# Kernel tuning notes

Measured on AMD Instinct MI355X. Metric: run time of the kernel, lower is better.

## Reference

```python
import jax, jax.numpy as jnp
import numpy as np

# Fixed problem geometry: B equal-sized graphs with contiguous node ids.
B, N, E, F_IN, H, C = 64, 1024, 655360, 128, 128, 10
K1 = int(np.ceil(0.8 * N))    # 820 nodes/graph kept by pool1
K2 = int(np.ceil(0.8 * K1))   # 656 nodes/graph kept by pool2


def setup_inputs() -> dict:
    key = jax.random.key(0)
    ks = jax.random.split(key, 12)
    x = jax.random.normal(ks[0], (B * N, F_IN), jnp.float32)
    # intra-graph random edges, E//B per graph
    e_per = E // B
    local = jax.random.randint(ks[1], (2, E), 0, N)
    off = jnp.repeat(jnp.arange(B, dtype=jnp.int32) * N, e_per)
    edge_index = (local + off[None, :]).astype(jnp.int32)
    batch = jnp.repeat(jnp.arange(B, dtype=jnp.int32), N)

    def lin(k, i, o):
        return jax.random.normal(k, (i, o), jnp.float32) / np.sqrt(i)

    return {
        "x": x, "edge_index": edge_index, "batch": batch,
        "Wl1": lin(ks[2], F_IN, H), "bl1": jnp.zeros((H,), jnp.float32), "Wr1": lin(ks[3], F_IN, H),
        "Wl2": lin(ks[4], H, H),    "bl2": jnp.zeros((H,), jnp.float32), "Wr2": lin(ks[5], H, H),
        "pw1": jax.random.normal(ks[6], (H,), jnp.float32) / np.sqrt(H),
        "pw2": jax.random.normal(ks[7], (H,), jnp.float32) / np.sqrt(H),
        "fW1": lin(ks[8], 2 * H, H), "fb1": jnp.zeros((H,), jnp.float32),
        "fW2": lin(ks[9], H, C),     "fb2": jnp.zeros((C,), jnp.float32),
    }


def _sage(x, src, dst, em, Wl, bl, Wr, n):
    # PyG SAGEConv (aggr='mean'): lin_l(mean_{j->i} x_j) + lin_r(x_i)
    msg = x[src] * em[:, None]                                   # [E, d]
    s = jax.ops.segment_sum(msg, dst, num_segments=n)            # [n, d]
    cnt = jax.ops.segment_sum(em, dst, num_segments=n)           # [n]
    mean = s / jnp.maximum(cnt, 1.0)[:, None]
    return mean @ Wl + bl + x @ Wr


def _topk_pool(x, src, dst, em, n_per, k, w):
    # PyG TopKPooling: score = tanh(x.w/||w||); keep top-k per graph; gate kept x by score.
    score = jnp.tanh(x @ w / jnp.linalg.norm(w))                 # [B*n_per]
    _, idx = jax.lax.top_k(score.reshape(B, n_per), k)           # [B, k]
    idx = jnp.sort(idx, axis=1)
    perm = (idx + (jnp.arange(B) * n_per)[:, None]).reshape(-1)  # global kept ids [B*k]
    nx = x[perm] * score[perm][:, None]
    # relabel edges; drop edges touching removed nodes via mask
    inv = jnp.full((B * n_per,), -1, jnp.int32).at[perm].set(jnp.arange(B * k, dtype=jnp.int32))
    ns, nd = inv[src], inv[dst]
    nm = em * (ns >= 0).astype(x.dtype) * (nd >= 0).astype(x.dtype)
    return nx, jnp.maximum(ns, 0), jnp.maximum(nd, 0), nm


def _readout(h, k):
    g = h.reshape(B, k, H)
    return jnp.concatenate([g.mean(axis=1), g.max(axis=1)], axis=1)  # [B, 2H]


def reference(x, edge_index, batch, Wl1, bl1, Wr1, Wl2, bl2, Wr2,
              pw1, pw2, fW1, fb1, fW2, fb2):
    src, dst = edge_index[0], edge_index[1]
    em = jnp.ones((E,), x.dtype)
    h = jax.nn.relu(_sage(x, src, dst, em, Wl1, bl1, Wr1, B * N))
    h, src, dst, em = _topk_pool(h, src, dst, em, N, K1, pw1)
    x1 = _readout(h, K1)
    h = jax.nn.relu(_sage(h, src, dst, em, Wl2, bl2, Wr2, B * K1))
    h, src, dst, em = _topk_pool(h, src, dst, em, K1, K2, pw2)
    x2 = _readout(h, K2)
    z = jax.nn.relu((x1 + x2) @ fW1 + fb1)
    # dropout is identity in eval mode
    return z @ fW2 + fb2
```

## Files before the change

### kernel.cpp

```cpp
#include <hip/hip_runtime.h>
#include <cstdint>
#include <cstddef>

namespace {

constexpr int kB    = 64;
constexpr int kN    = 1024;
constexpr int kE    = 655360;
constexpr int kEper = kE / kB;
constexpr int kH    = 128;
constexpr int kK1   = 820;
constexpr int kK2   = 656;
constexpr int kM1   = kB * kN;
constexpr int kM2   = kB * kK1;
constexpr int kM3   = kB * kK2;
constexpr int kRChunks = 16;

typedef __attribute__((ext_vector_type(8))) short bf16x8;
typedef __attribute__((ext_vector_type(4))) float f32x4;

__device__ inline ushort f2bf(float f) {
  uint u = __float_as_uint(f);
  return (ushort)((u + 0x7fffu + ((u >> 16) & 1u)) >> 16);
}
__device__ inline float bf2f(ushort s) { return __uint_as_float(((uint)s) << 16); }

__device__ inline void cvt4(const float* f, uint* hh, uint* ll) {
#pragma unroll
  for (int i = 0; i < 2; ++i) {
    uint h;
    asm("v_cvt_pk_bf16_f32 %0, %1, %2" : "=v"(h) : "v"(f[2 * i]), "v"(f[2 * i + 1]));
    const float r0 = __uint_as_float(h << 16);
    const float r1 = __uint_as_float(h & 0xFFFF0000u);
    const float d0 = f[2 * i] - r0;
    const float d1 = f[2 * i + 1] - r1;
    uint l;
    asm("v_cvt_pk_bf16_f32 %0, %1, %2" : "=v"(l) : "v"(d0), "v"(d1));
    hh[i] = h; ll[i] = l;
  }
}

__device__ inline void llds16(const void* g, void* l) {
  __builtin_amdgcn_global_load_lds(
      (const __attribute__((address_space(1))) void*)g,
      (__attribute__((address_space(3))) void*)l, 16, 0, 0);
}

__device__ inline int block_scan_1024(int v, int* wsum ) {
  const int lane = threadIdx.x & 63;
  const int w    = threadIdx.x >> 6;
#pragma unroll
  for (int off = 1; off < 64; off <<= 1) {
    const int n = __shfl_up(v, off);
    if (lane >= off) v += n;
  }
  if (lane == 63) wsum[w] = v;
  __syncthreads();
  if (w == 0) {
    int s = (lane < 16) ? wsum[lane] : 0;
#pragma unroll
    for (int off = 1; off < 16; off <<= 1) {
      const int n = __shfl_up(s, off);
      if (lane >= off) s += n;
    }
    if (lane < 16) wsum[lane] = s;
  }
  __syncthreads();
  if (w > 0) v += wsum[w - 1];
  return v;
}

__global__ __launch_bounds__(1024)
void build_prep(const int* __restrict__ src, const int* __restrict__ dst,
                int* __restrict__ coff, int* __restrict__ ccur,
                int* __restrict__ ent,
                const float* __restrict__ Wl1, const float* __restrict__ Wr1,
                const float* __restrict__ Wl2, const float* __restrict__ Wr2,
                const float* __restrict__ pw1, const float* __restrict__ pw2,
                ushort* __restrict__ W1h, ushort* __restrict__ W1l,
                ushort* __restrict__ W2h, ushort* __restrict__ W2l,
                float* __restrict__ pwn1, float* __restrict__ pwn2) {
  const int b   = blockIdx.x;
  const int tid = threadIdx.x;
  if (b >= 128) {
    if (tid >= 256) return;
    const float* pw = (tid < 128) ? pw1 : pw2;
    float* o        = (tid < 128) ? pwn1 : pwn2;
    const int j = tid & 127;
    float sum = 0.0f;
    for (int k = 0; k < 128; ++k) { const float v = pw[k]; sum += v * v; }
    o[j] = pw[j] / sqrtf(sum);
    return;
  }
  if (b >= 64) {
    const int ob  = (b - 64) * 4 + (tid >> 8);
    const bool l2 = ob >= 128;
    const int idx = (ob & 127) * 256 + (tid & 255);
    const int n = idx >> 8, k = idx & 255;
    const float* Wl = l2 ? Wl2 : Wl1;
    const float* Wr = l2 ? Wr2 : Wr1;
    const float w = (k < 128) ? Wl[k * kH + n] : Wr[(k - 128) * kH + n];
    const ushort h = f2bf(w);
    (l2 ? W2h : W1h)[n * 256 + k] = h;
    (l2 ? W2l : W1l)[n * 256 + k] = f2bf(w - bf2f(h));
    return;
  }
  __shared__ int cnt[1024];
  __shared__ int wsum[16];
  const int g = b;
  const int ebase = g * kEper;
  cnt[tid] = 0;
  __syncthreads();
  for (int e = tid; e < kEper; e += 1024)
    atomicAdd(&cnt[dst[ebase + e] & (kN - 1)], 1);
  __syncthreads();
  const int dg   = cnt[tid];
  const int incl = block_scan_1024(dg, wsum);
  const int start = ebase + incl - dg;
  coff[g * kN + tid] = start;
  ccur[g * kN + tid] = start + dg;
  __syncthreads();
  cnt[tid] = start;
  __syncthreads();
  for (int e = tid; e < kEper; e += 1024) {
    const int d   = dst[ebase + e] & (kN - 1);
    const int pos = atomicAdd(&cnt[d], 1);
    ent[pos] = src[ebase + e] & (kN - 1);
  }
}

__global__ __launch_bounds__(1024, 8)
void gather1_lds(const float* __restrict__ feat, const int* __restrict__ ent,
                 const int* __restrict__ off, const int* __restrict__ cursor,
                 float* __restrict__ aggout) {
  __shared__ float cache[1024 * 16];
  const int xcd   = blockIdx.x & 7;
  const int local = blockIdx.x >> 3;
  const int graph = xcd * 8 + (local >> 3);
  const int chunk = local & 7;
  const int tid   = threadIdx.x;
  const int wid   = tid >> 6;
  const int gbase = graph << 10;

#pragma unroll
  for (int ps = 0; ps < 4; ++ps) {
    const int row = ps * 256 + (tid >> 2);
    const int q   = (tid & 3) * 4;
    llds16(feat + (size_t)(gbase + row) * kH + chunk * 16 + q,
           cache + ps * 4096 + wid * 256);
  }
  __syncthreads();

  const int grp = tid >> 2;
  const int q4  = (tid & 3) * 4;

  for (int it = 0; it < 4; ++it) {
    const int lnode = it * 256 + grp;
    const int node  = gbase + lnode;
    const int o0 = off[node];
    const int o1 = cursor[node];
    const int deg = o1 - o0;
    float4 acc = make_float4(0.f, 0.f, 0.f, 0.f);
    int pf[4];
#pragma unroll
    for (int i = 0; i < 4; ++i) pf[i] = (o0 + i < o1) ? ent[o0 + i] : 0;
    for (int eb = 0; eb < deg; eb += 4) {
      int nx[4];
#pragma unroll
      for (int i = 0; i < 4; ++i) {
        const int idx = o0 + eb + 4 + i;
        nx[i] = (idx < o1) ? ent[idx] : 0;
      }
#pragma unroll
      for (int i = 0; i < 4; ++i) {
        const float m = (eb + i < deg) ? 1.0f : 0.0f;
        const float4 v = *(const float4*)&cache[pf[i] * 16 + q4];
        acc.x = fmaf(v.x, m, acc.x);
        acc.y = fmaf(v.y, m, acc.y);
        acc.z = fmaf(v.z, m, acc.z);
        acc.w = fmaf(v.w, m, acc.w);
      }
#pragma unroll
      for (int i = 0; i < 4; ++i) pf[i] = nx[i];
    }
    const float r = 1.0f / fmaxf((float)deg, 1.0f);
    const f32x4 res = {acc.x * r, acc.y * r, acc.z * r, acc.w * r};
    __builtin_nontemporal_store(res, (f32x4*)(aggout + (size_t)node * kH + chunk * 16 + q4));
  }
}

__global__ __launch_bounds__(1024, 8)
void gather2_lds(const float* __restrict__ feat, const int* __restrict__ ent,
                 const int* __restrict__ off, const int* __restrict__ cursor,
                 const int* __restrict__ perm, const float* __restrict__ gsg,
                 float* __restrict__ aggout,
                 float* __restrict__ psumg, float* __restrict__ pmaxg) {
  __shared__ float cache[1024 * 16];
  __shared__ float gs[1024];
  __shared__ float rps[16][16], rpm[16][16];
  const int xcd   = blockIdx.x & 7;
  const int local = blockIdx.x >> 3;
  const int graph = xcd * 8 + (local >> 3);
  const int chunk = local & 7;
  const int tid   = threadIdx.x;
  const int wid   = tid >> 6;
  const int gbase = graph << 10;

#pragma unroll
  for (int ps = 0; ps < 4; ++ps) {
    const int row = ps * 256 + (tid >> 2);
    const int q   = (tid & 3) * 4;
    llds16(feat + (size_t)(gbase + row) * kH + chunk * 16 + q,
           cache + ps * 4096 + wid * 256);
  }
  gs[tid] = gsg[gbase + tid];
  __syncthreads();

  const int grp = tid >> 2;
  const int q4  = (tid & 3) * 4;

  for (int it = 0; it < 4; ++it) {
    const int lnode = it * 256 + grp;
    int o0 = 0, o1 = 0;
    if (lnode < kK1) {
      const int orig = perm[graph * kK1 + lnode];
      o0 = off[orig];
      o1 = cursor[orig];
    }
    const int deg = o1 - o0;
    float4 acc = make_float4(0.f, 0.f, 0.f, 0.f);
    int cnt = 0;
    int pf[4];
#pragma unroll
    for (int i = 0; i < 4; ++i) pf[i] = (o0 + i < o1) ? ent[o0 + i] : 0;
    for (int eb = 0; eb < deg; eb += 4) {
      int nx[4];
#pragma unroll
      for (int i = 0; i < 4; ++i) {
        const int idx = o0 + eb + 4 + i;
        nx[i] = (idx < o1) ? ent[idx] : 0;
      }
#pragma unroll
      for (int i = 0; i < 4; ++i) {
        const float raw  = gs[pf[i]];
        const bool  kept = (raw > 0.5f) && (eb + i < deg);
        const float s    = kept ? raw - 2.0f : 0.0f;
        cnt += kept ? 1 : 0;
        const float4 v = *(const float4*)&cache[pf[i] * 16 + q4];
        acc.x = fmaf(v.x, s, acc.x);
        acc.y = fmaf(v.y, s, acc.y);
        acc.z = fmaf(v.z, s, acc.z);
        acc.w = fmaf(v.w, s, acc.w);
      }
#pragma unroll
      for (int i = 0; i < 4; ++i) pf[i] = nx[i];
    }
    const float r = 1.0f / fmaxf((float)cnt, 1.0f);
    const f32x4 res = {acc.x * r, acc.y * r, acc.z * r, acc.w * r};
    if (lnode < kK1)
      __builtin_nontemporal_store(res,
          (f32x4*)(aggout + (size_t)(graph * kK1 + lnode) * kH + chunk * 16 + q4));
  }

  __syncthreads();
  const int rcol = tid & 15;
  const int rseg = tid >> 4;
  float rs = 0.0f, rm = -1e30f;
#pragma unroll
  for (int i = 0; i < 16; ++i) {
    const int row = rseg * 16 + i;
    const float raw = gs[row];
    if (raw > 0.5f) {
      const float v = cache[row * 16 + rcol] * (raw - 2.0f);
      rs += v;
      rm = fmaxf(rm, v);
    }
  }
  rs += __shfl_xor(rs, 16); rs += __shfl_xor(rs, 32);
  rm = fmaxf(rm, __shfl_xor(rm, 16)); rm = fmaxf(rm, __shfl_xor(rm, 32));
  if ((tid & 48) == 0) { rps[wid][rcol] = rs; rpm[wid][rcol] = rm; }
  __syncthreads();
  if (tid < 16) {
    float ts = 0.0f, tm = -1e30f;
#pragma unroll
    for (int w = 0; w < 16; ++w) { ts += rps[w][tid]; tm = fmaxf(tm, rpm[w][tid]); }
    psumg[graph * kH + chunk * 16 + tid] = ts;
    pmaxg[graph * kH + chunk * 16 + tid] = tm;
  }
}

__global__ __launch_bounds__(256)
void sage_gemm_mfma(const float* __restrict__ meanb, const float* __restrict__ xsrc,
                    const int* __restrict__ perm, const float* __restrict__ gsc,
                    const ushort* __restrict__ WTh, const ushort* __restrict__ WTl,
                    const float* __restrict__ bias, const float* __restrict__ pwn,
                    float* __restrict__ outp, float* __restrict__ scr) {
  __shared__ __align__(16) ushort aH[64][32];
  __shared__ __align__(16) ushort aL[64][32];
  __shared__ __align__(16) ushort wHs[128][32];
  __shared__ __align__(16) ushort wLs[128][32];
  __shared__ float sdot[64][2];
  const int tid  = threadIdx.x;
  const int wid  = tid >> 6;
  const int lane = tid & 63;
  const int quad = lane >> 4;
  const int l16  = lane & 15;
  const int rowbase = blockIdx.x * 64;
  const int wr = (wid >> 1) * 32;
  const int wc = (wid & 1) * 64;

  const int n0a = wid * 32;
  const int n0b = wid * 32 + 16;
  const int wrowa = (n0a + (lane >> 2)) * 256 + (lane & 3) * 8;
  const int wrowb = (n0b + (lane >> 2)) * 256 + (lane & 3) * 8;

  int srow1[2]; float scl1[2];
#pragma unroll
  for (int i = 0; i < 2; ++i) {
    const int grow = rowbase + ((tid + i * 256) >> 3);
    srow1[i] = grow; scl1[i] = 1.0f;
    if (perm) { srow1[i] = perm[grow]; scl1[i] = gsc[grow]; }
  }

  f32x4 acc[2][4];
#pragma unroll
  for (int a = 0; a < 2; ++a)
#pragma unroll
    for (int b = 0; b < 4; ++b) acc[a][b] = (f32x4){0.f, 0.f, 0.f, 0.f};

  for (int s = 0; s < 8; ++s) {
    const bool ismean = s < 4;
    const float* sp = ismean ? meanb : xsrc;
    const int kbase = s * 32;
    const int kloc  = ismean ? kbase : kbase - 128;
#pragma unroll
    for (int i = 0; i < 2; ++i) {
      const int p   = tid + i * 256;
      const int row = p >> 3;
      const int k4  = (p & 7) * 4;
      const int srow   = ismean ? (rowbase + row) : srow1[i];
      const float scale = ismean ? 1.0f : scl1[i];
      const float4 v = *(const float4*)(sp + (size_t)srow * kH + kloc + k4);
      float f[4] = {v.x * scale, v.y * scale, v.z * scale, v.w * scale};
      uint hh[2], ll[2];
      cvt4(f, hh, ll);
      *(uint2*)&aH[row][k4] = make_uint2(hh[0], hh[1]);
      *(uint2*)&aL[row][k4] = make_uint2(ll[0], ll[1]);
    }
    llds16(WTh + wrowa + kbase, &wHs[n0a][0]);
    llds16(WTh + wrowb + kbase, &wHs[n0b][0]);
    llds16(WTl + wrowa + kbase, &wLs[n0a][0]);
    llds16(WTl + wrowb + kbase, &wLs[n0b][0]);
    __syncthreads();
    bf16x8 afh[2], afl[2];
#pragma unroll
    for (int rt = 0; rt < 2; ++rt) {
      afh[rt] = *(const bf16x8*)&aH[wr + rt * 16 + l16][quad * 8];
      afl[rt] = *(const bf16x8*)&aL[wr + rt * 16 + l16][quad * 8];
    }
#pragma unroll
    for (int ct = 0; ct < 4; ++ct) {
      const bf16x8 bh = *(const bf16x8*)&wHs[wc + ct * 16 + l16][quad * 8];
      const bf16x8 bl = *(const bf16x8*)&wLs[wc + ct * 16 + l16][quad * 8];
#pragma unroll
      for (int rt = 0; rt < 2; ++rt) {
        acc[rt][ct] = __builtin_amdgcn_mfma_f32_16x16x32_bf16(afh[rt], bh, acc[rt][ct], 0, 0, 0);
        acc[rt][ct] = __builtin_amdgcn_mfma_f32_16x16x32_bf16(afh[rt], bl, acc[rt][ct], 0, 0, 0);
        acc[rt][ct] = __builtin_amdgcn_mfma_f32_16x16x32_bf16(afl[rt], bh, acc[rt][ct], 0, 0, 0);
      }
    }
    __syncthreads();
  }
  float bv[4], pwv[4];
#pragma unroll
  for (int ct = 0; ct < 4; ++ct) {
    const int col = wc + ct * 16 + l16;
    bv[ct]  = bias[col];
    pwv[ct] = pwn[col];
  }
  float dot[2][4];
#pragma unroll
  for (int rt = 0; rt < 2; ++rt)
#pragma unroll
    for (int reg = 0; reg < 4; ++reg) dot[rt][reg] = 0.0f;
#pragma unroll
  for (int ct = 0; ct < 4; ++ct) {
    const int col = wc + ct * 16 + l16;
#pragma unroll
    for (int rt = 0; rt < 2; ++rt) {
#pragma unroll
      for (int reg = 0; reg < 4; ++reg) {
        const int row = rowbase + wr + rt * 16 + quad * 4 + reg;
        const float o = fmaxf(acc[rt][ct][reg] + bv[ct], 0.0f);
        outp[(size_t)row * kH + col] = o;
        dot[rt][reg] += o * pwv[ct];
      }
    }
  }
#pragma unroll
  for (int rt = 0; rt < 2; ++rt) {
#pragma unroll
    for (int reg = 0; reg < 4; ++reg) {
      float d = dot[rt][reg];
      d += __shfl_xor(d, 1);
      d += __shfl_xor(d, 2);
      d += __shfl_xor(d, 4);
      d += __shfl_xor(d, 8);
      if (l16 == 0) sdot[wr + rt * 16 + quad * 4 + reg][wc >> 6] = d;
    }
  }
  __syncthreads();
  if (tid < 64) scr[rowbase + tid] = tanhf(sdot[tid][0] + sdot[tid][1]);
}

__global__ __launch_bounds__(1024)
void rank_compact(const float* __restrict__ scr, int n_per, int K,
                  int* __restrict__ perm, float* __restrict__ gsc,
                  float* __restrict__ gsg) {
  __shared__ int hist[256];
  __shared__ int wsum[16];
  __shared__ uint bT;
  __shared__ int bRem;
  const int g = blockIdx.x, tid = threadIdx.x;
  const float sc = (tid < n_per) ? scr[g * n_per + tid] : -3e30f;
  const uint bits = __float_as_uint(sc);
  const uint key = (bits & 0x80000000u) ? ~bits : (bits | 0x80000000u);

  uint prefix = 0;
  int rem = K;
#pragma unroll
  for (int shift = 24; shift >= 0; shift -= 8) {
    if (tid < 256) hist[tid] = 0;
    __syncthreads();
    const uint mask = (shift == 24) ? 0u : (0xFFFFFFFFu << (shift + 8));
    if ((key & mask) == prefix)
      atomicAdd(&hist[(key >> shift) & 255], 1);
    __syncthreads();
    if (tid < 64) {
      const int h0 = hist[4 * tid + 0], h1 = hist[4 * tid + 1];
      const int h2 = hist[4 * tid + 2], h3 = hist[4 * tid + 3];
      const int loc = h0 + h1 + h2 + h3;
      int suf = loc;
#pragma unroll
      for (int d = 1; d < 64; d <<= 1) {
        const int o = __shfl_down(suf, d);
        if (tid + d < 64) suf += o;
      }
      const int above = suf - loc;
      int hs[5];
      hs[4] = above;
      hs[3] = above + h3;
      hs[2] = hs[3] + h2;
      hs[1] = hs[2] + h1;
      hs[0] = hs[1] + h0;
#pragma unroll
      for (int q = 0; q < 4; ++q) {
        if (hs[q] >= rem && hs[q + 1] < rem) {
          bT   = prefix | ((uint)(4 * tid + q) << shift);
          bRem = rem - hs[q + 1];
        }
      }
    }
    __syncthreads();
    prefix = bT;
    rem    = bRem;
  }
  const int gt = (key > prefix) ? 1 : 0;
  const int eq = (key == prefix) ? 1 : 0;
  const int incl = block_scan_1024((gt << 11) | eq, wsum);
  const int excl = incl - ((gt << 11) | eq);
  const int gt_excl = excl >> 11;
  const int eq_excl = excl & 2047;
  const int keep = (tid < n_per) && (gt || (eq && eq_excl < rem));
  if (keep) {
    const int pos = gt_excl + min(eq_excl, rem);
    perm[g * K + pos] = g * n_per + tid;
    gsc[g * K + pos]  = sc;
  }
  if (gsg) gsg[g * kN + tid] = keep ? sc + 2.0f : 0.0f;
}

__global__ __launch_bounds__(256)
void readout_part(const float* __restrict__ h, const int* __restrict__ perm,
                  const float* __restrict__ gsc, int K,
                  float* __restrict__ psum, float* __restrict__ pmax) {
  const int g     = blockIdx.x >> 4;
  const int chunk = blockIdx.x & (kRChunks - 1);
  const int j     = threadIdx.x & 127;
  const int part  = threadIdx.x >> 7;
  const int rows  = (K + kRChunks - 1) / kRChunks;
  const int r0 = chunk * rows;
  const int r1 = min(r0 + rows, K);
  float sum = 0.0f, mx = -1e30f;
  int r = r0 + part;
  if (r < r1) {
    int   row = perm[g * K + r];
    float sc  = gsc[g * K + r];
    while (r < r1) {
      const int rn = r + 2;
      int   row_n = 0;
      float sc_n  = 0.0f;
      if (rn < r1) { row_n = perm[g * K + rn]; sc_n = gsc[g * K + rn]; }
      const float v = h[(size_t)row * kH + j] * sc;
      sum += v;
      mx = fmaxf(mx, v);
      row = row_n; sc = sc_n; r = rn;
    }
  }
  __shared__ float ss[2][128], sm[2][128];
  ss[part][j] = sum;
  sm[part][j] = mx;
  __syncthreads();
  if (part == 0) {
    sum += ss[1][j];
    mx = fmaxf(mx, sm[1][j]);
    psum[(size_t)blockIdx.x * 128 + j] = sum;
    pmax[(size_t)blockIdx.x * 128 + j] = mx;
  }
}

__global__ __launch_bounds__(128)
void final_mlp(const float* __restrict__ ps1, const float* __restrict__ pm1,
               const float* __restrict__ ps2, const float* __restrict__ pm2,
               const float* __restrict__ fW1, const float* __restrict__ fb1,
               const float* __restrict__ fW2, const float* __restrict__ fb2,
               float* __restrict__ out) {
  __shared__ float xx[256];
  __shared__ float z[128];
  const int g = blockIdx.x, tid = threadIdx.x;
  const float s1 = ps1[(size_t)g * 128 + tid];
  const float m1 = pm1[(size_t)g * 128 + tid];
  float s2 = 0.f, m2 = -1e30f;
#pragma unroll
  for (int c = 0; c < kRChunks; ++c) {
    s2 += ps2[(size_t)(g * kRChunks + c) * 128 + tid];
    m2 = fmaxf(m2, pm2[(size_t)(g * kRChunks + c) * 128 + tid]);
  }
  xx[tid]       = s1 / (float)kK1 + s2 / (float)kK2;
  xx[tid + 128] = m1 + m2;
  __syncthreads();
  float a = fb1[tid];
  for (int k = 0; k < 256; ++k) a += xx[k] * fW1[k * 128 + tid];
  z[tid] = fmaxf(a, 0.0f);
  __syncthreads();
  if (tid < 10) {
    float o = fb2[tid];
    for (int k = 0; k < 128; ++k) o += z[k] * fW2[k * 10 + tid];
    out[g * 10 + tid] = o;
  }
}

}

extern "C" void kernel_launch(void* const* d_in, const int* in_sizes, int n_in,
                              void* d_out, int out_size, void* d_ws, size_t ws_size,
                              hipStream_t stream) {
  const float* x   = (const float*)d_in[0];
  const int*   ei  = (const int*)d_in[1];
  const float* Wl1 = (const float*)d_in[3];
  const float* bl1 = (const float*)d_in[4];
  const float* Wr1 = (const float*)d_in[5];
  const float* Wl2 = (const float*)d_in[6];
  const float* bl2 = (const float*)d_in[7];
  const float* Wr2 = (const float*)d_in[8];
  const float* pw1 = (const float*)d_in[9];
  const float* pw2 = (const float*)d_in[10];
  const float* fW1 = (const float*)d_in[11];
  const float* fb1 = (const float*)d_in[12];
  const float* fW2 = (const float*)d_in[13];
  const float* fb2 = (const float*)d_in[14];
  const int* src = ei;
  const int* dst = ei + kE;
  (void)in_sizes; (void)n_in; (void)out_size; (void)ws_size;

  char* wsb = (char*)d_ws;
  size_t off_b = 0;
  auto alloc = [&](size_t bytes) {
    void* p = wsb + off_b;
    off_b += (bytes + 255) & ~(size_t)255;
    return p;
  };
  float* bufA = (float*)alloc((size_t)kM1 * kH * 4);
  float* bufB = (float*)alloc((size_t)kM1 * kH * 4);
  float* bufC = (float*)alloc((size_t)kM2 * kH * 4);
  int*   coff = (int*)alloc((size_t)kM1 * 4);
  int*   ccur = (int*)alloc((size_t)kM1 * 4);
  int*   ent  = (int*)alloc((size_t)kE * 4);
  float* scr  = (float*)alloc((size_t)kM1 * 4);
  float* gsg  = (float*)alloc((size_t)kM1 * 4);
  int*   perm1= (int*)alloc((size_t)kM2 * 4);
  float* gsc1 = (float*)alloc((size_t)kM2 * 4);
  int*   perm2= (int*)alloc((size_t)kM3 * 4);
  float* gsc2 = (float*)alloc((size_t)kM3 * 4);
  float* psum1= (float*)alloc((size_t)kB * 128 * 4);
  float* pmax1= (float*)alloc((size_t)kB * 128 * 4);
  float* psum2= (float*)alloc((size_t)kB * kRChunks * 128 * 4);
  float* pmax2= (float*)alloc((size_t)kB * kRChunks * 128 * 4);
  ushort* wt1h = (ushort*)alloc((size_t)128 * 256 * 2);
  ushort* wt1l = (ushort*)alloc((size_t)128 * 256 * 2);
  ushort* wt2h = (ushort*)alloc((size_t)128 * 256 * 2);
  ushort* wt2l = (ushort*)alloc((size_t)128 * 256 * 2);
  float* pwn1 = (float*)alloc(128 * 4);
  float* pwn2 = (float*)alloc(128 * 4);

  build_prep<<<129, 1024, 0, stream>>>(src, dst, coff, ccur, ent,
                                       Wl1, Wr1, Wl2, Wr2, pw1, pw2,
                                       wt1h, wt1l, wt2h, wt2l, pwn1, pwn2);

  gather1_lds<<<kB * 8, 1024, 0, stream>>>(x, ent, coff, ccur, bufA);
  sage_gemm_mfma<<<kM1 / 64, 256, 0, stream>>>(bufA, x, nullptr, nullptr,
                                               wt1h, wt1l, bl1, pwn1, bufB, scr);
  rank_compact<<<kB, 1024, 0, stream>>>(scr, kN, kK1, perm1, gsc1, gsg);

  gather2_lds<<<kB * 8, 1024, 0, stream>>>(bufB, ent, coff, ccur, perm1, gsg,
                                           bufA, psum1, pmax1);
  sage_gemm_mfma<<<kM2 / 64, 256, 0, stream>>>(bufA, bufB, perm1, gsc1,
                                               wt2h, wt2l, bl2, pwn2, bufC, scr);
  rank_compact<<<kB, 1024, 0, stream>>>(scr, kK1, kK2, perm2, gsc2, nullptr);
  readout_part<<<kB * kRChunks, 256, 0, stream>>>(bufC, perm2, gsc2, kK2, psum2, pmax2);

  final_mlp<<<kB, 128, 0, stream>>>(psum1, pmax1, psum2, pmax2,
                                    fW1, fb1, fW2, fb2, (float*)d_out);
}
```

Before: 250.1 us.

## Fuse second top-k selection, readout and final MLP into one kernel

The second rank_compact, readout_part and final_mlp launches are replaced by a single per-graph kernel. It radix-selects the top-k scores, marks kept nodes in LDS, and accumulates the mean/max readout directly from h2 without building perm/gsc arrays. It then runs the MLP in the same block. This removes two kernel launches and the intermediate global buffers. In exchange the readout runs on only 64 blocks instead of 1024, which lowers parallelism for the h2 reads.

```diff
diff --git a/kernel.cpp b/kernel.cpp
--- a/kernel.cpp
+++ b/kernel.cpp
@@ -13,8 +13,6 @@
 constexpr int kK2   = 656;
 constexpr int kM1   = kB * kN;
 constexpr int kM2   = kB * kK1;
-constexpr int kM3   = kB * kK2;
-constexpr int kRChunks = 16;
 
 typedef __attribute__((ext_vector_type(8))) short bf16x8;
 typedef __attribute__((ext_vector_type(4))) float f32x4;
@@ -68,6 +66,58 @@
   __syncthreads();
   if (w > 0) v += wsum[w - 1];
   return v;
+}
+
+__device__ inline void radix_select(uint key, int K, int* hist, uint* bTp,
+                                    int* bRemp, uint& T, int& rem_out) {
+  const int tid = threadIdx.x;
+  uint prefix = 0;
+  int rem = K;
+#pragma unroll
+  for (int shift = 24; shift >= 0; shift -= 8) {
+    if (tid < 256) hist[tid] = 0;
+    __syncthreads();
+    const uint mask = (shift == 24) ? 0u : (0xFFFFFFFFu << (shift + 8));
+    if ((key & mask) == prefix)
+      atomicAdd(&hist[(key >> shift) & 255], 1);
+    __syncthreads();
+    if (tid < 64) {
+      const int h0 = hist[4 * tid + 0], h1 = hist[4 * tid + 1];
+      const int h2 = hist[4 * tid + 2], h3 = hist[4 * tid + 3];
+      const int loc = h0 + h1 + h2 + h3;
+      int suf = loc;
+#pragma unroll
+      for (int d = 1; d < 64; d <<= 1) {
+        const int o = __shfl_down(suf, d);
+        if (tid + d < 64) suf += o;
+      }
+      const int above = suf - loc;
+      int hs[5];
+      hs[4] = above;
+      hs[3] = above + h3;
+      hs[2] = hs[3] + h2;
+      hs[1] = hs[2] + h1;
+      hs[0] = hs[1] + h0;
+#pragma unroll
+      for (int q = 0; q < 4; ++q) {
+        if (hs[q] >= rem && hs[q + 1] < rem) {
+          *bTp   = prefix | ((uint)(4 * tid + q) << shift);
+          *bRemp = rem - hs[q + 1];
+        }
+      }
+    }
+    __syncthreads();
+    prefix = *bTp;
+    rem    = *bRemp;
+    __syncthreads();
+  }
+  T = prefix;
+  rem_out = rem;
+}
+
+__device__ inline uint score_key(float sc) {
+  const uint bits = __float_as_uint(sc);
+  return (bits & 0x80000000u) ? ~bits : (bits | 0x80000000u);
 }
 
 __global__ __launch_bounds__(1024)
@@ -423,50 +473,13 @@
   __shared__ int bRem;
   const int g = blockIdx.x, tid = threadIdx.x;
   const float sc = (tid < n_per) ? scr[g * n_per + tid] : -3e30f;
-  const uint bits = __float_as_uint(sc);
-  const uint key = (bits & 0x80000000u) ? ~bits : (bits | 0x80000000u);
-
-  uint prefix = 0;
-  int rem = K;
-#pragma unroll
-  for (int shift = 24; shift >= 0; shift -= 8) {
-    if (tid < 256) hist[tid] = 0;
-    __syncthreads();
-    const uint mask = (shift == 24) ? 0u : (0xFFFFFFFFu << (shift + 8));
-    if ((key & mask) == prefix)
-      atomicAdd(&hist[(key >> shift) & 255], 1);
-    __syncthreads();
-    if (tid < 64) {
-      const int h0 = hist[4 * tid + 0], h1 = hist[4 * tid + 1];
-      const int h2 = hist[4 * tid + 2], h3 = hist[4 * tid + 3];
-      const int loc = h0 + h1 + h2 + h3;
-      int suf = loc;
-#pragma unroll
-      for (int d = 1; d < 64; d <<= 1) {
-        const int o = __shfl_down(suf, d);
-        if (tid + d < 64) suf += o;
-      }
-      const int above = suf - loc;
-      int hs[5];
-      hs[4] = above;
-      hs[3] = above + h3;
-      hs[2] = hs[3] + h2;
-      hs[1] = hs[2] + h1;
-      hs[0] = hs[1] + h0;
-#pragma unroll
-      for (int q = 0; q < 4; ++q) {
-        if (hs[q] >= rem && hs[q + 1] < rem) {
-          bT   = prefix | ((uint)(4 * tid + q) << shift);
-          bRem = rem - hs[q + 1];
-        }
-      }
-    }
-    __syncthreads();
-    prefix = bT;
-    rem    = bRem;
-  }
-  const int gt = (key > prefix) ? 1 : 0;
-  const int eq = (key == prefix) ? 1 : 0;
+  const uint key = score_key(sc);
+
+  uint T; int rem;
+  radix_select(key, K, hist, &bT, &bRem, T, rem);
+
+  const int gt = (key > T) ? 1 : 0;
+  const int eq = (key == T) ? 1 : 0;
   const int incl = block_scan_1024((gt << 11) | eq, wsum);
   const int excl = incl - ((gt << 11) | eq);
   const int gt_excl = excl >> 11;
@@ -480,68 +493,65 @@
   if (gsg) gsg[g * kN + tid] = keep ? sc + 2.0f : 0.0f;
 }
 
-__global__ __launch_bounds__(256)
-void readout_part(const float* __restrict__ h, const int* __restrict__ perm,
-                  const float* __restrict__ gsc, int K,
-                  float* __restrict__ psum, float* __restrict__ pmax) {
-  const int g     = blockIdx.x >> 4;
-  const int chunk = blockIdx.x & (kRChunks - 1);
-  const int j     = threadIdx.x & 127;
-  const int part  = threadIdx.x >> 7;
-  const int rows  = (K + kRChunks - 1) / kRChunks;
-  const int r0 = chunk * rows;
-  const int r1 = min(r0 + rows, K);
-  float sum = 0.0f, mx = -1e30f;
-  int r = r0 + part;
-  if (r < r1) {
-    int   row = perm[g * K + r];
-    float sc  = gsc[g * K + r];
-    while (r < r1) {
-      const int rn = r + 2;
-      int   row_n = 0;
-      float sc_n  = 0.0f;
-      if (rn < r1) { row_n = perm[g * K + rn]; sc_n = gsc[g * K + rn]; }
-      const float v = h[(size_t)row * kH + j] * sc;
-      sum += v;
-      mx = fmaxf(mx, v);
-      row = row_n; sc = sc_n; r = rn;
-    }
-  }
-  __shared__ float ss[2][128], sm[2][128];
-  ss[part][j] = sum;
-  sm[part][j] = mx;
-  __syncthreads();
-  if (part == 0) {
-    sum += ss[1][j];
-    mx = fmaxf(mx, sm[1][j]);
-    psum[(size_t)blockIdx.x * 128 + j] = sum;
-    pmax[(size_t)blockIdx.x * 128 + j] = mx;
-  }
-}
-
-__global__ __launch_bounds__(128)
-void final_mlp(const float* __restrict__ ps1, const float* __restrict__ pm1,
-               const float* __restrict__ ps2, const float* __restrict__ pm2,
-               const float* __restrict__ fW1, const float* __restrict__ fb1,
-               const float* __restrict__ fW2, const float* __restrict__ fb2,
-               float* __restrict__ out) {
+__global__ __launch_bounds__(1024)
+void final_fused(const float* __restrict__ scr, const float* __restrict__ h2,
+                 const float* __restrict__ ps1, const float* __restrict__ pm1,
+                 const float* __restrict__ fW1, const float* __restrict__ fb1,
+                 const float* __restrict__ fW2, const float* __restrict__ fb2,
+                 float* __restrict__ out) {
+  __shared__ int hist[256];
+  __shared__ int wsum[16];
+  __shared__ uint bT;
+  __shared__ int bRem;
+  __shared__ float ls[1024];
+  __shared__ float ss[8][128], sm[8][128];
   __shared__ float xx[256];
   __shared__ float z[128];
   const int g = blockIdx.x, tid = threadIdx.x;
-  const float s1 = ps1[(size_t)g * 128 + tid];
-  const float m1 = pm1[(size_t)g * 128 + tid];
-  float s2 = 0.f, m2 = -1e30f;
-#pragma unroll
-  for (int c = 0; c < kRChunks; ++c) {
-    s2 += ps2[(size_t)(g * kRChunks + c) * 128 + tid];
-    m2 = fmaxf(m2, pm2[(size_t)(g * kRChunks + c) * 128 + tid]);
-  }
-  xx[tid]       = s1 / (float)kK1 + s2 / (float)kK2;
-  xx[tid + 128] = m1 + m2;
-  __syncthreads();
-  float a = fb1[tid];
-  for (int k = 0; k < 256; ++k) a += xx[k] * fW1[k * 128 + tid];
-  z[tid] = fmaxf(a, 0.0f);
+  const int n_per = kK1, K = kK2;
+
+  const float sc = (tid < n_per) ? scr[g * n_per + tid] : -3e30f;
+  const uint key = score_key(sc);
+  uint T; int rem;
+  radix_select(key, K, hist, &bT, &bRem, T, rem);
+  const int gt = (key > T) ? 1 : 0;
+  const int eq = (key == T) ? 1 : 0;
+  const int eq_incl = block_scan_1024(eq, wsum);
+  const int eq_excl = eq_incl - eq;
+  const int keep = (tid < n_per) && (gt || (eq && eq_excl < rem));
+  ls[tid] = keep ? sc + 2.0f : 0.0f;
+  __syncthreads();
+
+  const int part = tid >> 7;
+  const int j    = tid & 127;
+  float sum = 0.0f, mx = -1e30f;
+  for (int i = part; i < n_per; i += 8) {
+    const float raw = ls[i];
+    if (raw > 0.5f) {
+      const float v = h2[(size_t)(g * kK1 + i) * kH + j] * (raw - 2.0f);
+      sum += v;
+      mx = fmaxf(mx, v);
+    }
+  }
+  ss[part][j] = sum;
+  sm[part][j] = mx;
+  __syncthreads();
+
+  if (tid < 128) {
+    float s2 = 0.0f, m2 = -1e30f;
+#pragma unroll
+    for (int p = 0; p < 8; ++p) { s2 += ss[p][tid]; m2 = fmaxf(m2, sm[p][tid]); }
+    const float s1 = ps1[(size_t)g * 128 + tid];
+    const float m1 = pm1[(size_t)g * 128 + tid];
+    xx[tid]       = s1 / (float)kK1 + s2 / (float)K;
+    xx[tid + 128] = m1 + m2;
+  }
+  __syncthreads();
+  if (tid < 128) {
+    float a = fb1[tid];
+    for (int k = 0; k < 256; ++k) a += xx[k] * fW1[k * 128 + tid];
+    z[tid] = fmaxf(a, 0.0f);
+  }
   __syncthreads();
   if (tid < 10) {
     float o = fb2[tid];
@@ -590,12 +600,8 @@
   float* gsg  = (float*)alloc((size_t)kM1 * 4);
   int*   perm1= (int*)alloc((size_t)kM2 * 4);
   float* gsc1 = (float*)alloc((size_t)kM2 * 4);
-  int*   perm2= (int*)alloc((size_t)kM3 * 4);
-  float* gsc2 = (float*)alloc((size_t)kM3 * 4);
   float* psum1= (float*)alloc((size_t)kB * 128 * 4);
   float* pmax1= (float*)alloc((size_t)kB * 128 * 4);
-  float* psum2= (float*)alloc((size_t)kB * kRChunks * 128 * 4);
-  float* pmax2= (float*)alloc((size_t)kB * kRChunks * 128 * 4);
   ushort* wt1h = (ushort*)alloc((size_t)128 * 256 * 2);
   ushort* wt1l = (ushort*)alloc((size_t)128 * 256 * 2);
   ushort* wt2h = (ushort*)alloc((size_t)128 * 256 * 2);
@@ -616,9 +622,7 @@
                                            bufA, psum1, pmax1);
   sage_gemm_mfma<<<kM2 / 64, 256, 0, stream>>>(bufA, bufB, perm1, gsc1,
                                                wt2h, wt2l, bl2, pwn2, bufC, scr);
-  rank_compact<<<kB, 1024, 0, stream>>>(scr, kK1, kK2, perm2, gsc2, nullptr);
-  readout_part<<<kB * kRChunks, 256, 0, stream>>>(bufC, perm2, gsc2, kK2, psum2, pmax2);
-
-  final_mlp<<<kB, 128, 0, stream>>>(psum1, pmax1, psum2, pmax2,
-                                    fW1, fb1, fW2, fb2, (float*)d_out);
-}
+
+  final_fused<<<kB, 1024, 0, stream>>>(scr, bufC, psum1, pmax1,
+                                       fW1, fb1, fW2, fb2, (float*)d_out);
+}
```

Measured after the change: 264.3 us. 1.06x slower.
